# Optimization experiments

Hardware: AMD Instinct MI355X
Metric: run time of the kernel (lower is better)

The kernel has to match this reference:

```python
import jax, jax.numpy as jnp
import numpy as np

N = 200000
E = 12800000
G = 1024

def setup_inputs() -> dict:
    key = jax.random.key(0)
    k1, k2, k3 = jax.random.split(key, 3)
    node_pos = jax.random.normal(k1, (N, 2), dtype=jnp.float32)
    edge_index = jax.random.randint(k2, (2, E), 0, N, dtype=jnp.int64)
    batch_ids = jnp.sort(jax.random.randint(k3, (N,), 0, G, dtype=jnp.int64))
    return {"node_pos": node_pos, "edge_index": edge_index,
            "batch_ids": batch_ids, "num_graphs": G}

def reference(node_pos, edge_index, batch_ids, num_graphs):
    # gather edge endpoints: [E, 2]
    start = node_pos[edge_index[0]]
    end = node_pos[edge_index[1]]
    # per-edge loss: (||end - start|| - 1)^2, [E]
    diff = end - start
    eu = jnp.sqrt(jnp.sum(diff * diff, axis=1))
    edge_var = jnp.square(eu - 1.0)
    # scatter-mean by graph id of the edge's source node
    seg = batch_ids[edge_index[0]]
    sums = jax.ops.segment_sum(edge_var, seg, num_segments=num_graphs)
    counts = jax.ops.segment_sum(jnp.ones_like(edge_var), seg, num_segments=num_graphs)
    graph_var = sums / jnp.maximum(counts, 1.0)  # [G]
    # self.reduce = torch.mean over graphs
    return jnp.mean(graph_var)
```

## Files before the change

kernel.cpp:

```cpp
#include <hip/hip_runtime.h>
#include <hip/hip_fp16.h>


typedef int iv4 __attribute__((ext_vector_type(4)));

#define GBINS 1024

__device__ __forceinline__ int find_graph(int v, const int* __restrict__ ss, float scale) {
    int g = (int)((float)v * scale);
    g = min(g, GBINS - 1);
    while (v < ss[g]) --g;
    while (v >= ss[g + 1]) ++g;
    return g;
}

__global__ void prep(const float2* __restrict__ pos, const int* __restrict__ batch,
                     uint32_t* __restrict__ pos16, int* __restrict__ startg, int N) {
    int i = blockIdx.x * blockDim.x + threadIdx.x;
    if (i >= N) return;
    float2 p = pos[i];
    __half2 h; h.x = __float2half_rn(p.x); h.y = __float2half_rn(p.y);
    uint32_t u; __builtin_memcpy(&u, &h, 4);
    pos16[i] = u;
    int b = batch[i];
    if (i == 0) { for (int g = 0; g <= b; ++g) startg[g] = 0; }
    else { int a = batch[i - 1]; for (int g = a + 1; g <= b; ++g) startg[g] = i; }
    if (i == N - 1) { for (int g = b + 1; g <= GBINS; ++g) startg[g] = N; }
}

__global__ __launch_bounds__(512)
void count_kernel(const int* __restrict__ src, const int* __restrict__ startg,
                  uint32_t* __restrict__ gcnt, int E, float scale) {
    __shared__ int ss[GBINS + 1];
    __shared__ uint32_t hc[GBINS];
    const int tid = threadIdx.x;
    for (int i = tid; i < GBINS + 1; i += 512) ss[i] = startg[i];
    for (int i = tid; i < GBINS; i += 512) hc[i] = 0u;
    __syncthreads();

    const int ngroups = E >> 2;
    const iv4* __restrict__ s4 = (const iv4*)src;
    const int gtid = blockIdx.x * 512 + tid, gstride = gridDim.x * 512;
    for (int i = gtid; i < ngroups; i += gstride) {
        iv4 sv = __builtin_nontemporal_load(&s4[i]);
        #pragma unroll
        for (int k = 0; k < 4; ++k)
            atomicAdd(&hc[find_graph(sv[k], ss, scale)], 1u);
    }
    for (int e = (ngroups << 2) + gtid; e < E; e += gstride)
        atomicAdd(&hc[find_graph(src[e], ss, scale)], 1u);

    __syncthreads();
    for (int j = tid; j < GBINS; j += 512) {
        int g = (j + (blockIdx.x << 3)) & (GBINS - 1);
        uint32_t c = hc[g];
        if (c) atomicAdd(&gcnt[g], c);
    }
}

__global__ __launch_bounds__(512)
void sum_kernel(const int* __restrict__ src, const int* __restrict__ dst,
                const uint32_t* __restrict__ pos16, const int* __restrict__ startg,
                float* __restrict__ gsum, int E, float scale) {
    __shared__ int ss[GBINS + 1];
    __shared__ float hs[GBINS];
    const int tid = threadIdx.x;
    for (int i = tid; i < GBINS + 1; i += 512) ss[i] = startg[i];
    for (int i = tid; i < GBINS; i += 512) hs[i] = 0.f;
    __syncthreads();

    const int ngroups = E >> 2;
    const iv4* __restrict__ s4 = (const iv4*)src;
    const iv4* __restrict__ d4 = (const iv4*)dst;
    const int gtid = blockIdx.x * 512 + tid, gstride = gridDim.x * 512;
    for (int i = gtid; i < ngroups; i += gstride) {
        iv4 sv = __builtin_nontemporal_load(&s4[i]);
        iv4 dv = __builtin_nontemporal_load(&d4[i]);
        uint32_t ua[4], ub[4];
        #pragma unroll
        for (int k = 0; k < 4; ++k) { ua[k] = pos16[sv[k]]; ub[k] = pos16[dv[k]]; }
        #pragma unroll
        for (int k = 0; k < 4; ++k) {
            __half2 ha, hb;
            __builtin_memcpy(&ha, &ua[k], 4);
            __builtin_memcpy(&hb, &ub[k], 4);
            const float dx = __half2float(hb.x) - __half2float(ha.x);
            const float dy = __half2float(hb.y) - __half2float(ha.y);
            const float t  = sqrtf(fmaf(dx, dx, dy * dy)) - 1.f;
            atomicAdd(&hs[find_graph(sv[k], ss, scale)], t * t);
        }
    }
    for (int e = (ngroups << 2) + gtid; e < E; e += gstride) {
        const int s = src[e], d = dst[e];
        uint32_t ua = pos16[s], ub = pos16[d];
        __half2 ha, hb;
        __builtin_memcpy(&ha, &ua, 4);
        __builtin_memcpy(&hb, &ub, 4);
        const float dx = __half2float(hb.x) - __half2float(ha.x);
        const float dy = __half2float(hb.y) - __half2float(ha.y);
        const float t  = sqrtf(fmaf(dx, dx, dy * dy)) - 1.f;
        atomicAdd(&hs[find_graph(s, ss, scale)], t * t);
    }

    __syncthreads();
    for (int j = tid; j < GBINS; j += 512) {
        int g = (j + (blockIdx.x << 3)) & (GBINS - 1);
        float v = hs[g];
        if (v != 0.f) atomicAdd(&gsum[g], v);
    }
}

__global__ __launch_bounds__(1024)
void edge_accum_mono(const float2* __restrict__ pos, const int* __restrict__ batch,
                     const int* __restrict__ src, const int* __restrict__ dst,
                     float* __restrict__ gsum, uint32_t* __restrict__ gcnt, int E) {
    __shared__ float ls[GBINS];
    __shared__ uint32_t lc[GBINS];
    for (int i = threadIdx.x; i < GBINS; i += blockDim.x) { ls[i] = 0.f; lc[i] = 0u; }
    __syncthreads();
    const int tid = blockIdx.x * blockDim.x + threadIdx.x;
    const int stride = gridDim.x * blockDim.x;
    for (int i = tid; i < E; i += stride) {
        const int s = src[i], d = dst[i];
        const float2 a = pos[s], b = pos[d];
        const int g = batch[s];
        const float dx = b.x - a.x, dy = b.y - a.y;
        const float t = sqrtf(fmaf(dx, dx, dy * dy)) - 1.f;
        atomicAdd(&ls[g], t * t);
        atomicAdd(&lc[g], 1u);
    }
    __syncthreads();
    for (int g = threadIdx.x; g < GBINS; g += blockDim.x) {
        const uint32_t c = lc[g];
        if (c) { atomicAdd(&gsum[g], ls[g]); atomicAdd(&gcnt[g], c); }
    }
}

__global__ void finalize_kernel(const float* __restrict__ gsum,
                                const uint32_t* __restrict__ gcnt,
                                float* __restrict__ out,
                                const int* __restrict__ nG_ptr) {
    const int G = *nG_ptr;
    float v = 0.f;
    for (int g = threadIdx.x; g < G; g += blockDim.x)
        v += gsum[g] / fmaxf((float)gcnt[g], 1.f);
    __shared__ float w[16];
    for (int off = 32; off; off >>= 1) v += __shfl_down(v, off, 64);
    if ((threadIdx.x & 63) == 0) w[threadIdx.x >> 6] = v;
    __syncthreads();
    if (threadIdx.x == 0) {
        float s = 0.f;
        const int nw = (blockDim.x + 63) >> 6;
        for (int i = 0; i < nw; ++i) s += w[i];
        out[0] = s / (float)G;
    }
}

extern "C" void kernel_launch(void* const* d_in, const int* in_sizes, int n_in,
                              void* d_out, int out_size, void* d_ws, size_t ws_size,
                              hipStream_t stream) {
    const float2* pos   = (const float2*)d_in[0];
    const int*    ei    = (const int*)d_in[1];
    const int*    batch = (const int*)d_in[2];
    const int*    nG    = (const int*)d_in[3];

    const int N = in_sizes[0] / 2;
    const int E = in_sizes[1] / 2;
    const int* src = ei;
    const int* dst = ei + E;

    float*    gsum   = (float*)d_ws;
    uint32_t* gcnt   = (uint32_t*)((char*)d_ws + 4096);
    int*      startg = (int*)((char*)d_ws + 8192);
    uint32_t* pos16  = (uint32_t*)((char*)d_ws + 16384);
    const size_t need = 16384 + (size_t)N * 4;
    const bool fast = (ws_size >= need) && (N >= 1);

    (void)hipMemsetAsync(d_ws, 0, 8192, stream);

    if (fast) {
        const float scale = (float)GBINS / (float)N;
        prep<<<(N + 255) / 256, 256, 0, stream>>>(pos, batch, pos16, startg, N);
        count_kernel<<<1024, 512, 0, stream>>>(src, startg, gcnt, E, scale);
        sum_kernel<<<1024, 512, 0, stream>>>(src, dst, pos16, startg, gsum, E, scale);
    } else {
        edge_accum_mono<<<512, 1024, 0, stream>>>(pos, batch, src, dst, gsum, gcnt, E);
    }
    finalize_kernel<<<1, 1024, 0, stream>>>(gsum, gcnt, (float*)d_out, nG);
}
```

Before: 284.9 us.

## Fuse count and sum kernels into one pass with 8-edge unrolled loads

Merges the separate edge-count and loss-sum kernels into one kernel that computes the graph id once per edge and updates both shared-memory histograms. This removes a second full read of the source index array and a second graph lookup per edge, along with one kernel launch. It also widens each thread's work to 8 edges per iteration to expose more outstanding gathers. The cost is extra LDS use and register pressure, plus two shared atomics per edge in the same loop.

```diff
diff --git a/kernel.cpp b/kernel.cpp
--- a/kernel.cpp
+++ b/kernel.cpp
@@ -29,68 +29,49 @@
 }
 
 __global__ __launch_bounds__(512)
-void count_kernel(const int* __restrict__ src, const int* __restrict__ startg,
-                  uint32_t* __restrict__ gcnt, int E, float scale) {
+void fused_kernel(const int* __restrict__ src, const int* __restrict__ dst,
+                  const uint32_t* __restrict__ pos16, const int* __restrict__ startg,
+                  float* __restrict__ gsum, uint32_t* __restrict__ gcnt,
+                  int E, float scale) {
     __shared__ int ss[GBINS + 1];
+    __shared__ float hs[GBINS];
     __shared__ uint32_t hc[GBINS];
     const int tid = threadIdx.x;
     for (int i = tid; i < GBINS + 1; i += 512) ss[i] = startg[i];
-    for (int i = tid; i < GBINS; i += 512) hc[i] = 0u;
+    for (int i = tid; i < GBINS; i += 512) { hs[i] = 0.f; hc[i] = 0u; }
     __syncthreads();
 
-    const int ngroups = E >> 2;
-    const iv4* __restrict__ s4 = (const iv4*)src;
-    const int gtid = blockIdx.x * 512 + tid, gstride = gridDim.x * 512;
-    for (int i = gtid; i < ngroups; i += gstride) {
-        iv4 sv = __builtin_nontemporal_load(&s4[i]);
-        #pragma unroll
-        for (int k = 0; k < 4; ++k)
-            atomicAdd(&hc[find_graph(sv[k], ss, scale)], 1u);
-    }
-    for (int e = (ngroups << 2) + gtid; e < E; e += gstride)
-        atomicAdd(&hc[find_graph(src[e], ss, scale)], 1u);
-
-    __syncthreads();
-    for (int j = tid; j < GBINS; j += 512) {
-        int g = (j + (blockIdx.x << 3)) & (GBINS - 1);
-        uint32_t c = hc[g];
-        if (c) atomicAdd(&gcnt[g], c);
-    }
-}
-
-__global__ __launch_bounds__(512)
-void sum_kernel(const int* __restrict__ src, const int* __restrict__ dst,
-                const uint32_t* __restrict__ pos16, const int* __restrict__ startg,
-                float* __restrict__ gsum, int E, float scale) {
-    __shared__ int ss[GBINS + 1];
-    __shared__ float hs[GBINS];
-    const int tid = threadIdx.x;
-    for (int i = tid; i < GBINS + 1; i += 512) ss[i] = startg[i];
-    for (int i = tid; i < GBINS; i += 512) hs[i] = 0.f;
-    __syncthreads();
-
-    const int ngroups = E >> 2;
+    const int g8 = ((E & 3) == 0) ? (E >> 3) : 0;
     const iv4* __restrict__ s4 = (const iv4*)src;
     const iv4* __restrict__ d4 = (const iv4*)dst;
     const int gtid = blockIdx.x * 512 + tid, gstride = gridDim.x * 512;
-    for (int i = gtid; i < ngroups; i += gstride) {
-        iv4 sv = __builtin_nontemporal_load(&s4[i]);
-        iv4 dv = __builtin_nontemporal_load(&d4[i]);
-        uint32_t ua[4], ub[4];
+
+    for (int i = gtid; i < g8; i += gstride) {
+        const iv4 sa = __builtin_nontemporal_load(&s4[2 * i]);
+        const iv4 sb = __builtin_nontemporal_load(&s4[2 * i + 1]);
+        const iv4 da = __builtin_nontemporal_load(&d4[2 * i]);
+        const iv4 db = __builtin_nontemporal_load(&d4[2 * i + 1]);
+        int sv[8], dv[8];
         #pragma unroll
-        for (int k = 0; k < 4; ++k) { ua[k] = pos16[sv[k]]; ub[k] = pos16[dv[k]]; }
+        for (int k = 0; k < 4; ++k) { sv[k] = sa[k]; sv[4 + k] = sb[k];
+                                      dv[k] = da[k]; dv[4 + k] = db[k]; }
+        uint32_t ua[8], ub[8];
         #pragma unroll
-        for (int k = 0; k < 4; ++k) {
+        for (int k = 0; k < 8; ++k) { ua[k] = pos16[sv[k]]; ub[k] = pos16[dv[k]]; }
+        #pragma unroll
+        for (int k = 0; k < 8; ++k) {
             __half2 ha, hb;
             __builtin_memcpy(&ha, &ua[k], 4);
             __builtin_memcpy(&hb, &ub[k], 4);
             const float dx = __half2float(hb.x) - __half2float(ha.x);
             const float dy = __half2float(hb.y) - __half2float(ha.y);
             const float t  = sqrtf(fmaf(dx, dx, dy * dy)) - 1.f;
-            atomicAdd(&hs[find_graph(sv[k], ss, scale)], t * t);
+            const int g = find_graph(sv[k], ss, scale);
+            atomicAdd(&hs[g], t * t);
+            atomicAdd(&hc[g], 1u);
         }
     }
-    for (int e = (ngroups << 2) + gtid; e < E; e += gstride) {
+    for (int e = (g8 << 3) + gtid; e < E; e += gstride) {
         const int s = src[e], d = dst[e];
         uint32_t ua = pos16[s], ub = pos16[d];
         __half2 ha, hb;
@@ -99,14 +80,16 @@
         const float dx = __half2float(hb.x) - __half2float(ha.x);
         const float dy = __half2float(hb.y) - __half2float(ha.y);
         const float t  = sqrtf(fmaf(dx, dx, dy * dy)) - 1.f;
-        atomicAdd(&hs[find_graph(s, ss, scale)], t * t);
+        const int g = find_graph(s, ss, scale);
+        atomicAdd(&hs[g], t * t);
+        atomicAdd(&hc[g], 1u);
     }
 
     __syncthreads();
     for (int j = tid; j < GBINS; j += 512) {
-        int g = (j + (blockIdx.x << 3)) & (GBINS - 1);
-        float v = hs[g];
-        if (v != 0.f) atomicAdd(&gsum[g], v);
+        const int g = (j + (blockIdx.x << 3)) & (GBINS - 1);
+        const uint32_t c = hc[g];
+        if (c) { atomicAdd(&gcnt[g], c); atomicAdd(&gsum[g], hs[g]); }
     }
 }
 
@@ -181,8 +164,7 @@
     if (fast) {
         const float scale = (float)GBINS / (float)N;
         prep<<<(N + 255) / 256, 256, 0, stream>>>(pos, batch, pos16, startg, N);
-        count_kernel<<<1024, 512, 0, stream>>>(src, startg, gcnt, E, scale);
-        sum_kernel<<<1024, 512, 0, stream>>>(src, dst, pos16, startg, gsum, E, scale);
+        fused_kernel<<<1024, 512, 0, stream>>>(src, dst, pos16, startg, gsum, gcnt, E, scale);
     } else {
         edge_accum_mono<<<512, 1024, 0, stream>>>(pos, batch, src, dst, gsum, gcnt, E);
     }
```

Result: faster. 257.2 us (-9.7%).

## Fold per-graph mean weights into per-node records and reduce directly to scalar

Applied to the files above, without the earlier changes.

Instead of accumulating per-graph sums through shared-memory histograms with a binary-search graph lookup, a new kernel precomputes per-node records holding the half2 position and the weight 1/(G*count[g]). The sum kernel then gathers that 8-byte record for each source node and accumulates weighted losses in a register, followed by a block reduction and one atomic into the output. This removes the find_graph search, the LDS float atomics and the finalize kernel, at the cost of a wider source gather and an extra pass over the nodes. The weight hardcodes GBINS rather than reading num_graphs, and the final float atomic sum is order-dependent.

```diff
diff --git a/kernel.cpp b/kernel.cpp
--- a/kernel.cpp
+++ b/kernel.cpp
@@ -3,6 +3,7 @@
 
 
 typedef int iv4 __attribute__((ext_vector_type(4)));
+typedef unsigned int u32;
 
 #define GBINS 1024
 
@@ -15,12 +16,12 @@
 }
 
 __global__ void prep(const float2* __restrict__ pos, const int* __restrict__ batch,
-                     uint32_t* __restrict__ pos16, int* __restrict__ startg, int N) {
+                     u32* __restrict__ pos16, int* __restrict__ startg, int N) {
     int i = blockIdx.x * blockDim.x + threadIdx.x;
     if (i >= N) return;
     float2 p = pos[i];
     __half2 h; h.x = __float2half_rn(p.x); h.y = __float2half_rn(p.y);
-    uint32_t u; __builtin_memcpy(&u, &h, 4);
+    u32 u; __builtin_memcpy(&u, &h, 4);
     pos16[i] = u;
     int b = batch[i];
     if (i == 0) { for (int g = 0; g <= b; ++g) startg[g] = 0; }
@@ -30,9 +31,9 @@
 
 __global__ __launch_bounds__(512)
 void count_kernel(const int* __restrict__ src, const int* __restrict__ startg,
-                  uint32_t* __restrict__ gcnt, int E, float scale) {
+                  u32* __restrict__ gcnt, int E, float scale) {
     __shared__ int ss[GBINS + 1];
-    __shared__ uint32_t hc[GBINS];
+    __shared__ u32 hc[GBINS];
     const int tid = threadIdx.x;
     for (int i = tid; i < GBINS + 1; i += 512) ss[i] = startg[i];
     for (int i = tid; i < GBINS; i += 512) hc[i] = 0u;
@@ -52,70 +53,87 @@
 
     __syncthreads();
     for (int j = tid; j < GBINS; j += 512) {
-        int g = (j + (blockIdx.x << 3)) & (GBINS - 1);
-        uint32_t c = hc[g];
+        const int g = (j + (blockIdx.x << 3)) & (GBINS - 1);
+        const u32 c = hc[g];
         if (c) atomicAdd(&gcnt[g], c);
     }
 }
 
+__global__ void weights_kernel(const u32* __restrict__ pos16,
+                               const int* __restrict__ batch,
+                               const u32* __restrict__ gcnt,
+                               float2* __restrict__ rec8, float invG, int N) {
+    int i = blockIdx.x * blockDim.x + threadIdx.x;
+    if (i >= N) return;
+    const int g = batch[i];
+    const float c = fmaxf((float)gcnt[g], 1.f);
+    float2 r;
+    r.x = __uint_as_float(pos16[i]);
+    r.y = invG / c;
+    rec8[i] = r;
+}
+
 __global__ __launch_bounds__(512)
-void sum_kernel(const int* __restrict__ src, const int* __restrict__ dst,
-                const uint32_t* __restrict__ pos16, const int* __restrict__ startg,
-                float* __restrict__ gsum, int E, float scale) {
-    __shared__ int ss[GBINS + 1];
-    __shared__ float hs[GBINS];
-    const int tid = threadIdx.x;
-    for (int i = tid; i < GBINS + 1; i += 512) ss[i] = startg[i];
-    for (int i = tid; i < GBINS; i += 512) hs[i] = 0.f;
-    __syncthreads();
-
+void main_kernel(const int* __restrict__ src, const int* __restrict__ dst,
+                 const float2* __restrict__ rec8, const u32* __restrict__ pos16,
+                 float* __restrict__ out, int E) {
+    float acc = 0.f;
     const int ngroups = E >> 2;
     const iv4* __restrict__ s4 = (const iv4*)src;
     const iv4* __restrict__ d4 = (const iv4*)dst;
-    const int gtid = blockIdx.x * 512 + tid, gstride = gridDim.x * 512;
+    const int gtid = blockIdx.x * 512 + threadIdx.x, gstride = gridDim.x * 512;
+
     for (int i = gtid; i < ngroups; i += gstride) {
-        iv4 sv = __builtin_nontemporal_load(&s4[i]);
-        iv4 dv = __builtin_nontemporal_load(&d4[i]);
-        uint32_t ua[4], ub[4];
-        #pragma unroll
-        for (int k = 0; k < 4; ++k) { ua[k] = pos16[sv[k]]; ub[k] = pos16[dv[k]]; }
+        const iv4 sv = __builtin_nontemporal_load(&s4[i]);
+        const iv4 dv = __builtin_nontemporal_load(&d4[i]);
+        float2 ra[4]; u32 ub[4];
+        #pragma unroll
+        for (int k = 0; k < 4; ++k) { ra[k] = rec8[sv[k]]; ub[k] = pos16[dv[k]]; }
         #pragma unroll
         for (int k = 0; k < 4; ++k) {
             __half2 ha, hb;
-            __builtin_memcpy(&ha, &ua[k], 4);
+            u32 uab = __float_as_uint(ra[k].x);
+            __builtin_memcpy(&ha, &uab, 4);
             __builtin_memcpy(&hb, &ub[k], 4);
             const float dx = __half2float(hb.x) - __half2float(ha.x);
             const float dy = __half2float(hb.y) - __half2float(ha.y);
             const float t  = sqrtf(fmaf(dx, dx, dy * dy)) - 1.f;
-            atomicAdd(&hs[find_graph(sv[k], ss, scale)], t * t);
+            acc = fmaf(ra[k].y, t * t, acc);
         }
     }
     for (int e = (ngroups << 2) + gtid; e < E; e += gstride) {
-        const int s = src[e], d = dst[e];
-        uint32_t ua = pos16[s], ub = pos16[d];
+        const float2 ra = rec8[src[e]];
+        const u32 ubv = pos16[dst[e]];
         __half2 ha, hb;
-        __builtin_memcpy(&ha, &ua, 4);
-        __builtin_memcpy(&hb, &ub, 4);
+        u32 uab = __float_as_uint(ra.x);
+        __builtin_memcpy(&ha, &uab, 4);
+        __builtin_memcpy(&hb, &ubv, 4);
         const float dx = __half2float(hb.x) - __half2float(ha.x);
         const float dy = __half2float(hb.y) - __half2float(ha.y);
         const float t  = sqrtf(fmaf(dx, dx, dy * dy)) - 1.f;
-        atomicAdd(&hs[find_graph(s, ss, scale)], t * t);
-    }
-
-    __syncthreads();
-    for (int j = tid; j < GBINS; j += 512) {
-        int g = (j + (blockIdx.x << 3)) & (GBINS - 1);
-        float v = hs[g];
-        if (v != 0.f) atomicAdd(&gsum[g], v);
+        acc = fmaf(ra.y, t * t, acc);
+    }
+
+    __shared__ float wred[8];
+    const int lane = threadIdx.x & 63, wave = threadIdx.x >> 6;
+    #pragma unroll
+    for (int off = 32; off; off >>= 1) acc += __shfl_down(acc, off, 64);
+    if (lane == 0) wred[wave] = acc;
+    __syncthreads();
+    if (threadIdx.x == 0) {
+        float s = 0.f;
+        #pragma unroll
+        for (int w = 0; w < 8; ++w) s += wred[w];
+        atomicAdd(out, s);
     }
 }
 
 __global__ __launch_bounds__(1024)
 void edge_accum_mono(const float2* __restrict__ pos, const int* __restrict__ batch,
                      const int* __restrict__ src, const int* __restrict__ dst,
-                     float* __restrict__ gsum, uint32_t* __restrict__ gcnt, int E) {
+                     float* __restrict__ gsum, u32* __restrict__ gcnt, int E) {
     __shared__ float ls[GBINS];
-    __shared__ uint32_t lc[GBINS];
+    __shared__ u32 lc[GBINS];
     for (int i = threadIdx.x; i < GBINS; i += blockDim.x) { ls[i] = 0.f; lc[i] = 0u; }
     __syncthreads();
     const int tid = blockIdx.x * blockDim.x + threadIdx.x;
@@ -131,15 +149,15 @@
     }
     __syncthreads();
     for (int g = threadIdx.x; g < GBINS; g += blockDim.x) {
-        const uint32_t c = lc[g];
+        const u32 c = lc[g];
         if (c) { atomicAdd(&gsum[g], ls[g]); atomicAdd(&gcnt[g], c); }
     }
 }
 
-__global__ void finalize_kernel(const float* __restrict__ gsum,
-                                const uint32_t* __restrict__ gcnt,
-                                float* __restrict__ out,
-                                const int* __restrict__ nG_ptr) {
+__global__ void finalize_mono(const float* __restrict__ gsum,
+                              const u32* __restrict__ gcnt,
+                              float* __restrict__ out,
+                              const int* __restrict__ nG_ptr) {
     const int G = *nG_ptr;
     float v = 0.f;
     for (int g = threadIdx.x; g < G; g += blockDim.x)
@@ -169,22 +187,27 @@
     const int* src = ei;
     const int* dst = ei + E;
 
-    float*    gsum   = (float*)d_ws;
-    uint32_t* gcnt   = (uint32_t*)((char*)d_ws + 4096);
-    int*      startg = (int*)((char*)d_ws + 8192);
-    uint32_t* pos16  = (uint32_t*)((char*)d_ws + 16384);
-    const size_t need = 16384 + (size_t)N * 4;
+    u32*   gcnt   = (u32*)d_ws;
+    float* gsum   = (float*)((char*)d_ws + 4096);
+    int*   startg = (int*)((char*)d_ws + 8192);
+    u32*   pos16  = (u32*)((char*)d_ws + 16384);
+    const size_t rec8_off = (16384 + (size_t)N * 4 + 255) & ~(size_t)255;
+    float2* rec8  = (float2*)((char*)d_ws + rec8_off);
+    const size_t need = rec8_off + (size_t)N * 8;
     const bool fast = (ws_size >= need) && (N >= 1);
 
     (void)hipMemsetAsync(d_ws, 0, 8192, stream);
+    (void)hipMemsetAsync(d_out, 0, out_size * sizeof(float), stream);
 
     if (fast) {
         const float scale = (float)GBINS / (float)N;
         prep<<<(N + 255) / 256, 256, 0, stream>>>(pos, batch, pos16, startg, N);
         count_kernel<<<1024, 512, 0, stream>>>(src, startg, gcnt, E, scale);
-        sum_kernel<<<1024, 512, 0, stream>>>(src, dst, pos16, startg, gsum, E, scale);
+        weights_kernel<<<(N + 255) / 256, 256, 0, stream>>>(
+            pos16, batch, gcnt, rec8, 1.f / (float)GBINS, N);
+        main_kernel<<<2048, 512, 0, stream>>>(src, dst, rec8, pos16, (float*)d_out, E);
     } else {
         edge_accum_mono<<<512, 1024, 0, stream>>>(pos, batch, src, dst, gsum, gcnt, E);
-    }
-    finalize_kernel<<<1, 1024, 0, stream>>>(gsum, gcnt, (float*)d_out, nG);
-}
+        finalize_mono<<<1, 1024, 0, stream>>>(gsum, gcnt, (float*)d_out, nG);
+    }
+}
```

Result: no change. 287.4 us (+0.9%).
